# Optimization experiments

Hardware: AMD Instinct MI355X
Metric: run time of the kernel (lower is better)

## Reference

```python
import jax, jax.numpy as jnp
import numpy as np

B, N, E, P, NH = 8, 1024, 768, 768, 12
HD = P // NH


def setup_inputs() -> dict:
    key = jax.random.key(0)
    ks = jax.random.split(key, 9)
    s = lambda k, sh: jax.random.normal(k, sh, dtype=jnp.float32) * 0.02
    return {
        "x": jax.random.normal(ks[0], (B, N, E), dtype=jnp.float32),
        "wq": s(ks[1], (E, P)), "bq": jnp.zeros((P,), jnp.float32),
        "wk": s(ks[2], (E, P)), "bk": jnp.zeros((P,), jnp.float32),
        "wv": s(ks[3], (E, P)), "bv": jnp.zeros((P,), jnp.float32),
        "wo": s(ks[4], (P, E)), "bo": jnp.zeros((E,), jnp.float32),
        "H": 32, "W": 32,
    }


def reference(x, wq, bq, wk, bk, wv, bv, wo, bo, H, W):
    b, n, _ = x.shape
    # QKV projections: [B,N,P] -> [B,NH,N,HD]
    def split_heads(t):
        return t.reshape(b, n, NH, HD).transpose(0, 2, 1, 3)
    q = split_heads(x @ wq + bq)
    k = split_heads(x @ wk + bk)
    v = split_heads(x @ wv + bv)
    # NOTE: original module applies NO 1/sqrt(head_dim) scaling.
    logits = jnp.einsum("bhqd,bhkd->bhqk", q, k)  # [B,NH,N,N]
    attn = jax.nn.softmax(logits, axis=-1)
    ctx = jnp.einsum("bhqk,bhkd->bhqd", attn, v)  # [B,NH,N,HD]
    ctx = ctx.transpose(0, 2, 1, 3).reshape(b, n, P)
    return ctx @ wo + bo
```

## Files before the change

### kernel.cpp

```cpp
#include <hip/hip_runtime.h>
#include <hip/hip_bf16.h>
#include <math.h>

#define B_   8
#define N_   1024
#define E_   768
#define P_   768
#define NH_  12
#define HD_  64
#define L2E  1.44269504088896340736f

typedef __attribute__((ext_vector_type(8))) short short8;
typedef __attribute__((ext_vector_type(4))) float f32x4;

__device__ inline void async16(void* lds, const void* g) {
    __builtin_amdgcn_global_load_lds(
        (const __attribute__((address_space(1))) void*)g,
        (__attribute__((address_space(3))) void*)lds, 16, 0, 0);
}

__device__ inline unsigned pkbf(float a, float b) {
    union { float f; unsigned u; } ua, ub;
    ua.f = a; ub.f = b;
    return __builtin_amdgcn_perm(ub.u, ua.u, 0x07060302u);
}

__global__ __launch_bounds__(256) void cvt_x(const float* __restrict__ x,
                                             __hip_bfloat16* __restrict__ xb, int n4) {
    int i = blockIdx.x * blockDim.x + threadIdx.x;
    const int stride = gridDim.x * blockDim.x;
    for (; i < n4; i += stride) {
        float4 f = ((const float4*)x)[i];
        union { __hip_bfloat16 h[4]; uint2 u; } pk;
        pk.h[0] = __float2bfloat16(f.x);
        pk.h[1] = __float2bfloat16(f.y);
        pk.h[2] = __float2bfloat16(f.z);
        pk.h[3] = __float2bfloat16(f.w);
        ((uint2*)xb)[i] = pk.u;
    }
}

__global__ __launch_bounds__(256) void cvt_tw(
    const float* __restrict__ W0, const float* __restrict__ W1,
    const float* __restrict__ W2, const float* __restrict__ W3,
    __hip_bfloat16* __restrict__ T0, __hip_bfloat16* __restrict__ T1,
    __hip_bfloat16* __restrict__ T2, __hip_bfloat16* __restrict__ T3) {
    const int z = blockIdx.z;
    const float* W = (z == 0) ? W0 : (z == 1) ? W1 : (z == 2) ? W2 : W3;
    __hip_bfloat16* T = (z == 0) ? T0 : (z == 1) ? T1 : (z == 2) ? T2 : T3;
    __shared__ float t[32][33];
    const int tx = threadIdx.x & 31, ty = threadIdx.x >> 5;
    const int n0 = blockIdx.x * 32, k0 = blockIdx.y * 32;
#pragma unroll
    for (int rr = 0; rr < 4; ++rr)
        t[ty + rr * 8][tx] = W[(k0 + ty + rr * 8) * 768 + n0 + tx];
    __syncthreads();
#pragma unroll
    for (int rr = 0; rr < 4; ++rr)
        T[(long)(n0 + ty + rr * 8) * 768 + k0 + tx] = __float2bfloat16(t[tx][ty + rr * 8]);
}

template <int NC>
__global__ __launch_bounds__(256) void gemm_core(
    const __hip_bfloat16* __restrict__ A0, const __hip_bfloat16* __restrict__ A1,
    const __hip_bfloat16* __restrict__ A2,
    const __hip_bfloat16* __restrict__ B01, const __hip_bfloat16* __restrict__ B2,
    const float* __restrict__ b0, const float* __restrict__ b1,
    const float* __restrict__ b2,
    void* __restrict__ C0, void* __restrict__ C1, void* __restrict__ C2,
    int fused) {
    constexpr int ABUF = 8192;
    constexpr int BBUF = NC * 64;
    constexpr int JT = NC / 32;
    __shared__ char As[2 * ABUF];
    __shared__ char Bs[2 * BBUF];

    const __hip_bfloat16* Arows;
    const __hip_bfloat16* Brows;
    const float* bias;
    void* Cout;
    int mode, rb, cb;
    if (fused) {
        const int xcd = blockIdx.x & 7, t = blockIdx.x >> 3;
        const int g = t % 18, yhi = t / 18;
        const int y = yhi * 8 + xcd;
        if (g < 12) {
            mode = 2;
            const int z = g / 6;
            rb = (g % 6) * 128; cb = y * 128;
            Arows = z ? A1 : A0; Brows = B01; bias = z ? b1 : b0; Cout = z ? C1 : C0;
        } else {
            mode = 1;
            rb = y * 128; cb = (g - 12) * 128;
            Arows = A2; Brows = B2; bias = b2; Cout = C2;
        }
    } else {
        mode = 3;
        const int xcd = blockIdx.x & 7, t = blockIdx.x >> 3;
        const int e = t % 6, thi = t / 6;
        const int tc = thi * 8 + xcd;
        rb = e * 128; cb = tc * NC;
        Arows = A0; Brows = B01; bias = b0; Cout = C0;
    }

    const int tid = threadIdx.x;
    const int lane = tid & 63;
    const int w = tid >> 6;
    const int l15 = lane & 15;
    const int quad = lane >> 4;
    const int mh = (w >> 1) * 64;
    const int nh = (w & 1) * (NC / 2);

    f32x4 acc[4][JT];
#pragma unroll
    for (int i = 0; i < 4; ++i)
#pragma unroll
        for (int j = 0; j < JT; ++j) acc[i][j] = (f32x4){0.f, 0.f, 0.f, 0.f};

    const int c1 = tid + 256;
    const int ar0 = tid >> 2, alc0 = (tid & 3) ^ ((ar0 >> 1) & 3);
    const int ar1 = c1 >> 2,  alc1 = (c1 & 3) ^ ((ar1 >> 1) & 3);
    const __hip_bfloat16* gA0 = Arows + (long)(rb + ar0) * 768 + alc0 * 8;
    const __hip_bfloat16* gA1 = Arows + (long)(rb + ar1) * 768 + alc1 * 8;
    const __hip_bfloat16* gB0 = Brows + (long)(cb + ar0) * 768 + alc0 * 8;
    const __hip_bfloat16* gB1 = (NC == 128) ? (Brows + (long)(cb + ar1) * 768 + alc1 * 8) : nullptr;

    async16(As + tid * 16, gA0);
    async16(As + c1 * 16, gA1);
    async16(Bs + tid * 16, gB0);
    if (NC == 128) async16(Bs + c1 * 16, gB1);

    for (int it = 0; it < 24; ++it) {
        const int boA = (it & 1) * ABUF, noA = ABUF - boA;
        const int boB = (it & 1) * BBUF, noB = BBUF - boB;
        __syncthreads();
        if (it + 1 < 24) {
            const int k1 = (it + 1) * 32;
            async16(As + noA + tid * 16, gA0 + k1);
            async16(As + noA + c1 * 16, gA1 + k1);
            async16(Bs + noB + tid * 16, gB0 + k1);
            if (NC == 128) async16(Bs + noB + c1 * 16, gB1 + k1);
        }

        short8 a[4], b[JT];
#pragma unroll
        for (int i = 0; i < 4; ++i) {
            const int row = mh + i * 16 + l15;
            a[i] = *(const short8*)(As + boA + row * 64 + (quad ^ ((row >> 1) & 3)) * 16);
        }
#pragma unroll
        for (int j = 0; j < JT; ++j) {
            const int row = nh + j * 16 + l15;
            b[j] = *(const short8*)(Bs + boB + row * 64 + (quad ^ ((row >> 1) & 3)) * 16);
        }
#pragma unroll
        for (int i = 0; i < 4; ++i)
#pragma unroll
            for (int j = 0; j < JT; ++j)
                acc[i][j] = __builtin_amdgcn_mfma_f32_16x16x32_bf16(a[i], b[j], acc[i][j], 0, 0, 0);
    }

    if (mode == 2) {
        __hip_bfloat16* O = (__hip_bfloat16*)Cout;
#pragma unroll
        for (int j = 0; j < JT; ++j) {
            const int n = cb + nh + j * 16 + l15;
            const int bb = n >> 10, nn = n & 1023;
#pragma unroll
            for (int i = 0; i < 4; ++i) {
                const int p0 = rb + mh + i * 16 + quad * 4;
                const int h = p0 >> 6, d0 = p0 & 63;
                const float4 bv = *(const float4*)(bias + p0);
                union { __hip_bfloat16 h4[4]; unsigned long long u; } pk;
                pk.h4[0] = __float2bfloat16(acc[i][j][0] + bv.x);
                pk.h4[1] = __float2bfloat16(acc[i][j][1] + bv.y);
                pk.h4[2] = __float2bfloat16(acc[i][j][2] + bv.z);
                pk.h4[3] = __float2bfloat16(acc[i][j][3] + bv.w);
                *(unsigned long long*)(O + (((long)(bb * NH_ + h)) * N_ + nn) * HD_ + d0) = pk.u;
            }
        }
    } else if (mode == 1) {
        __hip_bfloat16* O = (__hip_bfloat16*)Cout;
#pragma unroll
        for (int j = 0; j < JT; ++j) {
            const int p = cb + nh + j * 16 + l15;
            const int h = p >> 6, d = p & 63;
            const float bv = bias[p];
#pragma unroll
            for (int i = 0; i < 4; ++i) {
                const int n0 = rb + mh + i * 16 + quad * 4;
                const int bb = n0 >> 10, nn = n0 & 1023;
                union { __hip_bfloat16 h4[4]; unsigned long long u; } pk;
#pragma unroll
                for (int r = 0; r < 4; ++r)
                    pk.h4[r] = __float2bfloat16(acc[i][j][r] + bv);
                *(unsigned long long*)(O + (((long)(bb * NH_ + h)) * HD_ + d) * N_ + nn) = pk.u;
            }
        }
    } else {
        float* O = (float*)Cout;
#pragma unroll
        for (int j = 0; j < JT; ++j) {
            const int n = cb + nh + j * 16 + l15;
#pragma unroll
            for (int i = 0; i < 4; ++i) {
                const int e0 = rb + mh + i * 16 + quad * 4;
                const float4 bv = *(const float4*)(bias + e0);
                float4 vo;
                vo.x = acc[i][j][0] + bv.x;
                vo.y = acc[i][j][1] + bv.y;
                vo.z = acc[i][j][2] + bv.z;
                vo.w = acc[i][j][3] + bv.w;
                *(float4*)(O + (long)n * 768 + e0) = vo;
            }
        }
    }
}

__global__ __launch_bounds__(256, 3) void attn_mfma(
    const __hip_bfloat16* __restrict__ Q, const __hip_bfloat16* __restrict__ K,
    const __hip_bfloat16* __restrict__ Vt, __hip_bfloat16* __restrict__ ctx) {
    __shared__ __hip_bfloat16 Ks[2 * 64 * 64];
    __shared__ __hip_bfloat16 Vs[2 * 64 * 64];

    const int tid = threadIdx.x;
    const int lane = tid & 63, w = tid >> 6;
    const int l15 = lane & 15, quad = lane >> 4;
    const int y3 = l15 & 7;

    const int bx = blockIdx.x;
    const int rr_ = bx & 7, t_ = bx >> 3;
    const int qb = t_ & 7, hi_ = t_ >> 3;
    const int H = hi_ * 8 + rr_;
    const int bz = H / 12, hy = H - bz * 12;
    const long headOff = (long)H * (N_ * HD_);
    const int qBase = qb * 128;

    short8 qf[2][2];
#pragma unroll
    for (int i = 0; i < 2; ++i)
#pragma unroll
        for (int ks = 0; ks < 2; ++ks)
            qf[i][ks] = *(const short8*)(Q + headOff +
                (long)(qBase + w * 32 + i * 16 + l15) * HD_ + ks * 32 + quad * 8);

    f32x4 o[4][2];
#pragma unroll
    for (int mt = 0; mt < 4; ++mt)
#pragma unroll
        for (int i = 0; i < 2; ++i) o[mt][i] = (f32x4){0.f, 0.f, 0.f, 0.f};
    f32x4 ol[2];
    ol[0] = (f32x4){0.f, 0.f, 0.f, 0.f};
    ol[1] = (f32x4){0.f, 0.f, 0.f, 0.f};
    const short8 onesv = (short8){0x3F80, 0x3F80, 0x3F80, 0x3F80,
                                  0x3F80, 0x3F80, 0x3F80, 0x3F80};

    const int p0 = tid, p1 = tid + 256;
    const int r0 = p0 >> 3, lc0 = (p0 & 7) ^ (r0 & 7);
    const int r1 = p1 >> 3, lc1 = (p1 & 7) ^ (r1 & 7);
    const __hip_bfloat16* gK0 = K + headOff + r0 * HD_ + lc0 * 8;
    const __hip_bfloat16* gK1 = K + headOff + r1 * HD_ + lc1 * 8;
    const __hip_bfloat16* gV0 = Vt + headOff + r0 * N_ + lc0 * 8;
    const __hip_bfloat16* gV1 = Vt + headOff + r1 * N_ + lc1 * 8;
    const int q0 = p0 * 16, q1 = p1 * 16;

    async16((char*)Ks + q0, gK0);
    async16((char*)Ks + q1, gK1);
    async16((char*)Vs + q0, gV0);
    async16((char*)Vs + q1, gV1);

    for (int it = 0; it < 16; ++it) {
        const int bo = (it & 1) * 8192;
        const int no = 8192 - bo;
        __syncthreads();
        if (it + 1 < 16) {
            const int j1 = (it + 1) * 64;
            async16((char*)Ks + no + q0, gK0 + (long)j1 * HD_);
            async16((char*)Ks + no + q1, gK1 + (long)j1 * HD_);
            async16((char*)Vs + no + q0, gV0 + j1);
            async16((char*)Vs + no + q1, gV1 + j1);
        }

        f32x4 sT[4][2];
#pragma unroll
        for (int n = 0; n < 4; ++n)
#pragma unroll
            for (int i = 0; i < 2; ++i) sT[n][i] = (f32x4){0.f, 0.f, 0.f, 0.f};
#pragma unroll
        for (int ks = 0; ks < 2; ++ks) {
            short8 kf[4];
#pragma unroll
            for (int n = 0; n < 4; ++n)
                kf[n] = *(const short8*)((char*)Ks + bo +
                    ((n * 16 + l15) * 64 + (((ks * 4 + quad) ^ y3) * 8)) * 2);
#pragma unroll
            for (int n = 0; n < 4; ++n)
#pragma unroll
                for (int i = 0; i < 2; ++i)
                    sT[n][i] = __builtin_amdgcn_mfma_f32_16x16x32_bf16(kf[n], qf[i][ks], sT[n][i], 0, 0, 0);
        }

        short8 pf[2][2];
#pragma unroll
        for (int i = 0; i < 2; ++i) {
            float pv[4][4];
#pragma unroll
            for (int n = 0; n < 4; ++n)
#pragma unroll
                for (int r = 0; r < 4; ++r)
                    pv[n][r] = __expf(sT[n][i][r] - 16.635532333438686f);
            union { unsigned u[4]; short8 v; } pk0, pk1;
            pk0.u[0] = pkbf(pv[0][0], pv[0][1]);
            pk0.u[1] = pkbf(pv[0][2], pv[0][3]);
            pk0.u[2] = pkbf(pv[1][0], pv[1][1]);
            pk0.u[3] = pkbf(pv[1][2], pv[1][3]);
            pk1.u[0] = pkbf(pv[2][0], pv[2][1]);
            pk1.u[1] = pkbf(pv[2][2], pv[2][3]);
            pk1.u[2] = pkbf(pv[3][0], pv[3][1]);
            pk1.u[3] = pkbf(pv[3][2], pv[3][3]);
            pf[i][0] = pk0.v;
            pf[i][1] = pk1.v;
        }

#pragma unroll
        for (int g = 0; g < 2; ++g) {
#pragma unroll
            for (int mt = 0; mt < 4; ++mt) {
                const int row = mt * 16 + l15;
                union { short s4[2][4]; short8 v; } vb;
#pragma unroll
                for (int h = 0; h < 2; ++h) {
                    const int chunk = g * 4 + h * 2 + (quad >> 1);
                    *(long*)vb.s4[h] = *(const long*)((char*)Vs + bo +
                        (row * 64 + ((chunk ^ y3) * 8 + (quad & 1) * 4)) * 2);
                }
#pragma unroll
                for (int i = 0; i < 2; ++i)
                    o[mt][i] = __builtin_amdgcn_mfma_f32_16x16x32_bf16(vb.v, pf[i][g], o[mt][i], 0, 0, 0);
            }
#pragma unroll
            for (int i = 0; i < 2; ++i)
                ol[i] = __builtin_amdgcn_mfma_f32_16x16x32_bf16(onesv, pf[i][g], ol[i], 0, 0, 0);
        }
    }

#pragma unroll
    for (int i = 0; i < 2; ++i) {
        const float inv = 1.0f / ol[i][0];
        const int q = qBase + w * 32 + i * 16 + l15;
        __hip_bfloat16* op = ctx + ((long)(bz * N_ + q)) * P_ + hy * HD_;
#pragma unroll
        for (int mt = 0; mt < 4; ++mt) {
            union { __hip_bfloat16 h[4]; unsigned long long u; } pk;
#pragma unroll
            for (int r = 0; r < 4; ++r)
                pk.h[r] = __float2bfloat16(o[mt][i][r] * inv);
            *(unsigned long long*)(op + mt * 16 + quad * 4) = pk.u;
        }
    }
}

extern "C" void kernel_launch(void* const* d_in, const int* in_sizes, int n_in,
                              void* d_out, int out_size, void* d_ws, size_t ws_size,
                              hipStream_t stream) {
    const float* x  = (const float*)d_in[0];
    const float* wq = (const float*)d_in[1];
    const float* bq = (const float*)d_in[2];
    const float* wk = (const float*)d_in[3];
    const float* bk = (const float*)d_in[4];
    const float* wv = (const float*)d_in[5];
    const float* bv = (const float*)d_in[6];
    const float* wo = (const float*)d_in[7];
    const float* bo = (const float*)d_in[8];
    float* out = (float*)d_out;

    char* p = (char*)d_ws;
    const long XB = (long)B_ * N_ * E_ * 2;
    const long WB = (long)E_ * P_ * 2;
    const long HB = (long)B_ * NH_ * N_ * HD_ * 2;
    __hip_bfloat16* xb  = (__hip_bfloat16*)p; p += XB;
    __hip_bfloat16* wqt = (__hip_bfloat16*)p; p += WB;
    __hip_bfloat16* wkt = (__hip_bfloat16*)p; p += WB;
    __hip_bfloat16* wvt = (__hip_bfloat16*)p; p += WB;
    __hip_bfloat16* wot = (__hip_bfloat16*)p; p += WB;
    __hip_bfloat16* qh  = (__hip_bfloat16*)p; p += HB;
    __hip_bfloat16* kh  = (__hip_bfloat16*)p; p += HB;
    __hip_bfloat16* vth = (__hip_bfloat16*)p; p += HB;
    __hip_bfloat16* ctxb = (__hip_bfloat16*)p; p += HB;

    cvt_x<<<2048, 256, 0, stream>>>(x, xb, (B_ * N_ * E_) / 4);
    cvt_tw<<<dim3(24, 24, 4), 256, 0, stream>>>(wq, wk, wv, wo, wqt, wkt, wvt, wot);

    gemm_core<128><<<dim3(1152), 256, 0, stream>>>(
        wqt, wkt, xb, xb, wvt, bq, bk, bv, qh, kh, vth, 1);

    attn_mfma<<<dim3(768), 256, 0, stream>>>(qh, kh, vth, ctxb);

    gemm_core<64><<<dim3(768), 256, 0, stream>>>(
        wot, wot, wot, ctxb, ctxb, bo, bo, bo, out, out, out, 0);
}
```

Before: 222.4 us.

## Triple-buffer LDS loads with one barrier per iteration and MFMA priority hints

Moves the GEMM and attention kernels from double to triple buffering. Loads now run two tiles ahead, and explicit vmcnt waits plus a single s_barrier replace __syncthreads, so a tile's global-to-LDS copy overlaps more compute. s_setprio brackets around the MFMA blocks favour matrix-issuing waves. This uses 50% more LDS per block, which may cut occupancy in attention (launch bound 3), and the hand-counted vmcnt values must match the number of outstanding loads.

```diff
diff --git a/kernel.cpp b/kernel.cpp
--- a/kernel.cpp
+++ b/kernel.cpp
@@ -72,8 +72,8 @@
     constexpr int ABUF = 8192;
     constexpr int BBUF = NC * 64;
     constexpr int JT = NC / 32;
-    __shared__ char As[2 * ABUF];
-    __shared__ char Bs[2 * BBUF];
+    __shared__ char As[3 * ABUF];
+    __shared__ char Bs[3 * BBUF];
 
     const __hip_bfloat16* Arows;
     const __hip_bfloat16* Brows;
@@ -129,17 +129,30 @@
     async16(As + c1 * 16, gA1);
     async16(Bs + tid * 16, gB0);
     if (NC == 128) async16(Bs + c1 * 16, gB1);
+    async16(As + ABUF + tid * 16, gA0 + 32);
+    async16(As + ABUF + c1 * 16, gA1 + 32);
+    async16(Bs + BBUF + tid * 16, gB0 + 32);
+    if (NC == 128) async16(Bs + BBUF + c1 * 16, gB1 + 32);
 
     for (int it = 0; it < 24; ++it) {
-        const int boA = (it & 1) * ABUF, noA = ABUF - boA;
-        const int boB = (it & 1) * BBUF, noB = BBUF - boB;
-        __syncthreads();
-        if (it + 1 < 24) {
-            const int k1 = (it + 1) * 32;
-            async16(As + noA + tid * 16, gA0 + k1);
-            async16(As + noA + c1 * 16, gA1 + k1);
-            async16(Bs + noB + tid * 16, gB0 + k1);
-            if (NC == 128) async16(Bs + noB + c1 * 16, gB1 + k1);
+        const int bi = it % 3;
+        const int boA = bi * ABUF;
+        const int boB = bi * BBUF;
+        if (it < 23) {
+            if (NC == 128) asm volatile("s_waitcnt vmcnt(4)" ::: "memory");
+            else           asm volatile("s_waitcnt vmcnt(3)" ::: "memory");
+        } else {
+            asm volatile("s_waitcnt vmcnt(0)" ::: "memory");
+        }
+        __builtin_amdgcn_s_barrier();
+        asm volatile("" ::: "memory");
+        if (it + 2 < 24) {
+            const int pb = (it + 2) % 3;
+            const int k2 = (it + 2) * 32;
+            async16(As + pb * ABUF + tid * 16, gA0 + k2);
+            async16(As + pb * ABUF + c1 * 16, gA1 + k2);
+            async16(Bs + pb * BBUF + tid * 16, gB0 + k2);
+            if (NC == 128) async16(Bs + pb * BBUF + c1 * 16, gB1 + k2);
         }
 
         short8 a[4], b[JT];
@@ -153,11 +166,13 @@
             const int row = nh + j * 16 + l15;
             b[j] = *(const short8*)(Bs + boB + row * 64 + (quad ^ ((row >> 1) & 3)) * 16);
         }
+        __builtin_amdgcn_s_setprio(1);
 #pragma unroll
         for (int i = 0; i < 4; ++i)
 #pragma unroll
             for (int j = 0; j < JT; ++j)
                 acc[i][j] = __builtin_amdgcn_mfma_f32_16x16x32_bf16(a[i], b[j], acc[i][j], 0, 0, 0);
+        __builtin_amdgcn_s_setprio(0);
     }
 
     if (mode == 2) {
@@ -220,8 +235,8 @@
 __global__ __launch_bounds__(256, 3) void attn_mfma(
     const __hip_bfloat16* __restrict__ Q, const __hip_bfloat16* __restrict__ K,
     const __hip_bfloat16* __restrict__ Vt, __hip_bfloat16* __restrict__ ctx) {
-    __shared__ __hip_bfloat16 Ks[2 * 64 * 64];
-    __shared__ __hip_bfloat16 Vs[2 * 64 * 64];
+    __shared__ __hip_bfloat16 Ks[3 * 64 * 64];
+    __shared__ __hip_bfloat16 Vs[3 * 64 * 64];
 
     const int tid = threadIdx.x;
     const int lane = tid & 63, w = tid >> 6;
@@ -243,6 +258,7 @@
         for (int ks = 0; ks < 2; ++ks)
             qf[i][ks] = *(const short8*)(Q + headOff +
                 (long)(qBase + w * 32 + i * 16 + l15) * HD_ + ks * 32 + quad * 8);
+    asm volatile("" :: "v"(qf[0][0]), "v"(qf[0][1]), "v"(qf[1][0]), "v"(qf[1][1]));
 
     f32x4 o[4][2];
 #pragma unroll
@@ -268,17 +284,24 @@
     async16((char*)Ks + q1, gK1);
     async16((char*)Vs + q0, gV0);
     async16((char*)Vs + q1, gV1);
+    async16((char*)Ks + 8192 + q0, gK0 + (long)64 * HD_);
+    async16((char*)Ks + 8192 + q1, gK1 + (long)64 * HD_);
+    async16((char*)Vs + 8192 + q0, gV0 + 64);
+    async16((char*)Vs + 8192 + q1, gV1 + 64);
 
     for (int it = 0; it < 16; ++it) {
-        const int bo = (it & 1) * 8192;
-        const int no = 8192 - bo;
-        __syncthreads();
-        if (it + 1 < 16) {
-            const int j1 = (it + 1) * 64;
-            async16((char*)Ks + no + q0, gK0 + (long)j1 * HD_);
-            async16((char*)Ks + no + q1, gK1 + (long)j1 * HD_);
-            async16((char*)Vs + no + q0, gV0 + j1);
-            async16((char*)Vs + no + q1, gV1 + j1);
+        const int bo = (it % 3) * 8192;
+        if (it < 15) asm volatile("s_waitcnt vmcnt(4)" ::: "memory");
+        else         asm volatile("s_waitcnt vmcnt(0)" ::: "memory");
+        __builtin_amdgcn_s_barrier();
+        asm volatile("" ::: "memory");
+        if (it + 2 < 16) {
+            const int po = ((it + 2) % 3) * 8192;
+            const long j1 = (long)(it + 2) * 64;
+            async16((char*)Ks + po + q0, gK0 + j1 * HD_);
+            async16((char*)Ks + po + q1, gK1 + j1 * HD_);
+            async16((char*)Vs + po + q0, gV0 + j1);
+            async16((char*)Vs + po + q1, gV1 + j1);
         }
 
         f32x4 sT[4][2];
@@ -293,11 +316,13 @@
             for (int n = 0; n < 4; ++n)
                 kf[n] = *(const short8*)((char*)Ks + bo +
                     ((n * 16 + l15) * 64 + (((ks * 4 + quad) ^ y3) * 8)) * 2);
+            __builtin_amdgcn_s_setprio(1);
 #pragma unroll
             for (int n = 0; n < 4; ++n)
 #pragma unroll
                 for (int i = 0; i < 2; ++i)
                     sT[n][i] = __builtin_amdgcn_mfma_f32_16x16x32_bf16(kf[n], qf[i][ks], sT[n][i], 0, 0, 0);
+            __builtin_amdgcn_s_setprio(0);
         }
 
         short8 pf[2][2];
@@ -334,9 +359,11 @@
                     *(long*)vb.s4[h] = *(const long*)((char*)Vs + bo +
                         (row * 64 + ((chunk ^ y3) * 8 + (quad & 1) * 4)) * 2);
                 }
+                __builtin_amdgcn_s_setprio(1);
 #pragma unroll
                 for (int i = 0; i < 2; ++i)
                     o[mt][i] = __builtin_amdgcn_mfma_f32_16x16x32_bf16(vb.v, pf[i][g], o[mt][i], 0, 0, 0);
+                __builtin_amdgcn_s_setprio(0);
             }
 #pragma unroll
             for (int i = 0; i < 2; ++i)
```

Measured after the change: 220.9 us. No clear change (-0.7%).
